# Performance work log

Measured on AMD Instinct MI355X. Metric: run time of the kernel, lower is better.

## Reference

```python
import jax, jax.numpy as jnp
import numpy as np

B, S, H, E, I_E, V = 4, 4096, 1024, 8, 512, 100000


def setup_inputs() -> dict:
    key = jax.random.key(0)
    k0, k1, k2, k3, k4, k5, k6 = jax.random.split(key, 7)
    hidden_states = jax.random.normal(k0, (B, S, H), dtype=jnp.float32)
    token_ids = jax.random.randint(k1, (B, S), 0, V, dtype=jnp.int64)
    mu = jax.random.normal(k2, (B, S, H), dtype=jnp.float32)
    # torch Linear(in,out,bias=False) weight is [out,in]; we store transposed [in,out]
    w_gate = jax.random.normal(k3, (E, H, I_E), dtype=jnp.float32) * 0.02
    w_up = jax.random.normal(k4, (E, H, I_E), dtype=jnp.float32) * 0.02
    w_down = jax.random.normal(k5, (E, I_E, H), dtype=jnp.float32) * 0.02
    # module zero-inits mu_router; use small random so the mu-override path is exercised
    mu_router_w = jax.random.normal(k6, (E, H), dtype=jnp.float32) * 0.02
    return {
        "hidden_states": hidden_states,
        "token_ids": token_ids,
        "mu": mu,
        "w_gate": w_gate,
        "w_up": w_up,
        "w_down": w_down,
        "mu_router_w": mu_router_w,
    }


def reference(hidden_states, token_ids, mu, w_gate, w_up, w_down, mu_router_w):
    num_experts = w_gate.shape[0]
    # deterministic token->expert mapping: token_id % num_experts (after clamp)
    tid = jnp.clip(token_ids, 0, V - 1)
    base_expert_ids = (tid % num_experts).astype(jnp.int32)  # [B,S]
    # mu-guided override: one_hot*10 + mu_logits, argmax
    mu_logits = jnp.einsum("bsh,eh->bse", mu, mu_router_w)
    base_one_hot = jax.nn.one_hot(base_expert_ids, num_experts, dtype=mu_logits.dtype)
    expert_ids = jnp.argmax(base_one_hot * 10.0 + mu_logits, axis=-1)  # [B,S]

    x = hidden_states.reshape(-1, H)          # [T,H], T=B*S
    eid = expert_ids.reshape(-1)              # [T]
    out = jnp.zeros_like(x)
    for e in range(num_experts):
        mask = (eid == e)[:, None]            # [T,1]
        g = x @ w_gate[e]                     # [T,I_E]
        u = x @ w_up[e]                       # [T,I_E]
        y = (jax.nn.silu(g) * u) @ w_down[e]  # [T,H] SwiGLU
        out = out + jnp.where(mask, y, 0.0)
    return out.reshape(hidden_states.shape)
```

## Files before the change

### kernel.cpp

```cpp
#include <hip/hip_runtime.h>
#include <stdint.h>

#define T_TOK   16384
#define H_DIM   1024
#define IE_DIM  512
#define E_NUM   8
#define V_MAX   100000

typedef __attribute__((ext_vector_type(8))) short bf16x8;
typedef __attribute__((ext_vector_type(4))) float f32x4;
typedef unsigned long long ull;

__device__ __forceinline__ unsigned short f2bf(float f) {
  union { float f; unsigned u; } v; v.f = f;
  unsigned r = v.u + 0x7fffu + ((v.u >> 16) & 1u);
  return (unsigned short)(r >> 16);
}

__device__ __forceinline__ void gload16(const void* g, void* l) {
  __builtin_amdgcn_global_load_lds(
      (const __attribute__((address_space(1))) unsigned int*)g,
      (__attribute__((address_space(3))) unsigned int*)(unsigned int)(uintptr_t)l,
      16, 0, 0);
}

__global__ __launch_bounds__(256) void k_route(
    const float* __restrict__ mu, const int* __restrict__ tok,
    const float* __restrict__ mrw, int* __restrict__ eid,
    int* __restrict__ blockCnt) {
  int wv = blockIdx.x * 4 + (threadIdx.x >> 6);
  int t0 = wv * 4;
  int lane = threadIdx.x & 63;
  const float4* mrw4 = (const float4*)mrw;

  __shared__ int cnt[8];
  if (threadIdx.x < 8) cnt[threadIdx.x] = 0;

  float acc[4][E_NUM];
#pragma unroll
  for (int i = 0; i < 4; i++)
#pragma unroll
    for (int e = 0; e < E_NUM; e++) acc[i][e] = 0.f;

#pragma unroll
  for (int j = 0; j < 4; j++) {
    int idx = lane + 64 * j;
    float4 wr[E_NUM];
#pragma unroll
    for (int e = 0; e < E_NUM; e++) wr[e] = mrw4[e * 256 + idx];
#pragma unroll
    for (int i = 0; i < 4; i++) {
      float4 m = ((const float4*)(mu + (size_t)(t0 + i) * H_DIM))[idx];
#pragma unroll
      for (int e = 0; e < E_NUM; e++)
        acc[i][e] += m.x * wr[e].x + m.y * wr[e].y + m.z * wr[e].z + m.w * wr[e].w;
    }
  }
#pragma unroll
  for (int i = 0; i < 4; i++)
#pragma unroll
    for (int e = 0; e < E_NUM; e++)
#pragma unroll
      for (int off = 32; off >= 1; off >>= 1)
        acc[i][e] += __shfl_xor(acc[i][e], off, 64);

  __syncthreads();
#pragma unroll
  for (int i = 0; i < 4; i++) {
    int tv = tok[t0 + i];
    if (tv < 0) tv = 0;
    if (tv > V_MAX - 1) tv = V_MAX - 1;
    int base = tv & 7;
    int best = 0; float bs = -1e30f;
#pragma unroll
    for (int e = 0; e < E_NUM; e++) {
      float s = acc[i][e] + (e == base ? 10.f : 0.f);
      if (s > bs) { bs = s; best = e; }
    }
    if (lane == i) {
      eid[t0 + i] = best;
      atomicAdd(&cnt[best], 1);
    }
  }
  __syncthreads();
  if (threadIdx.x < 8) blockCnt[blockIdx.x * 8 + threadIdx.x] = cnt[threadIdx.x];
}

__global__ __launch_bounds__(1024) void k_scan2(
    const int* __restrict__ blockCnt, int* __restrict__ blockBase,
    int* __restrict__ offsets, int* __restrict__ tileOff) {
  int b = threadIdx.x;
  __shared__ ull s0[1024], s1[1024];
  __shared__ int offL[8];
  const int4* p = (const int4*)(blockCnt + b * 8);
  int4 x0 = p[0], x1 = p[1];
  int c[8] = {x0.x, x0.y, x0.z, x0.w, x1.x, x1.y, x1.z, x1.w};
  ull v0 = (ull)c[0] | ((ull)c[1] << 16) | ((ull)c[2] << 32) | ((ull)c[3] << 48);
  ull v1 = (ull)c[4] | ((ull)c[5] << 16) | ((ull)c[6] << 32) | ((ull)c[7] << 48);
  s0[b] = v0; s1[b] = v1;
  __syncthreads();
  for (int st = 1; st < 1024; st <<= 1) {
    ull a0 = 0, a1 = 0;
    if (b >= st) { a0 = s0[b - st]; a1 = s1[b - st]; }
    __syncthreads();
    v0 += a0; v1 += a1;
    s0[b] = v0; s1[b] = v1;
    __syncthreads();
  }
  if (b == 1023) {
    int tot[8];
#pragma unroll
    for (int e = 0; e < 4; e++) tot[e] = (int)((v0 >> (16 * e)) & 0xFFFF);
#pragma unroll
    for (int e = 0; e < 4; e++) tot[4 + e] = (int)((v1 >> (16 * e)) & 0xFFFF);
    int s = 0, ts = 0;
    for (int e = 0; e < E_NUM; e++) {
      offsets[e] = s; offL[e] = s; tileOff[e] = ts;
      s += tot[e];
      ts += (tot[e] + 127) >> 7;
    }
    offsets[E_NUM] = s; tileOff[E_NUM] = ts;
  }
  __syncthreads();
  int be[8];
#pragma unroll
  for (int e = 0; e < 4; e++)
    be[e] = offL[e] + (int)((v0 >> (16 * e)) & 0xFFFF) - c[e];
#pragma unroll
  for (int e = 0; e < 4; e++)
    be[4 + e] = offL[4 + e] + (int)((v1 >> (16 * e)) & 0xFFFF) - c[4 + e];
  int4* q = (int4*)(blockBase + b * 8);
  q[0] = make_int4(be[0], be[1], be[2], be[3]);
  q[1] = make_int4(be[4], be[5], be[6], be[7]);
}

__global__ __launch_bounds__(256) void k_gather(
    const float* __restrict__ hs, const int* __restrict__ eid,
    const int* __restrict__ blockBase, int* __restrict__ tokofrow,
    unsigned short* __restrict__ Xs) {
  int b = blockIdx.x;
  int tid = threadIdx.x;
  __shared__ int eL[16];
  __shared__ int posL[16];
  if (tid < 16) eL[tid] = eid[b * 16 + tid];
  __syncthreads();
  if (tid < 16) {
    int e = eL[tid];
    int r = 0;
    for (int j = 0; j < tid; j++) r += (eL[j] == e);
    int pos = blockBase[b * 8 + e] + r;
    posL[tid] = pos;
    tokofrow[pos] = b * 16 + tid;
  }
  __syncthreads();
  int w = tid >> 6, lane = tid & 63;
#pragma unroll
  for (int i = 0; i < 4; i++) {
    int li = w * 4 + i;
    int t = b * 16 + li;
    int pos = posL[li];
    const float4* src = (const float4*)(hs + (size_t)t * H_DIM);
    unsigned short* drow = Xs + (size_t)pos * H_DIM;
#pragma unroll
    for (int j = 0; j < 4; j++) {
      float4 v = src[lane + 64 * j];
      ushort4 bb;
      bb.x = f2bf(v.x); bb.y = f2bf(v.y); bb.z = f2bf(v.z); bb.w = f2bf(v.w);
      *(ushort4*)(drow + (lane + 64 * j) * 4) = bb;
    }
  }
}

__global__ __launch_bounds__(256) void k_transpose3(
    const float* __restrict__ wg, const float* __restrict__ wu,
    const float* __restrict__ wd, unsigned short* __restrict__ WgT,
    unsigned short* __restrict__ WuT, unsigned short* __restrict__ WdT) {
  int sel = blockIdx.x >> 10;
  int blk = blockIdx.x & 1023;
  const float* src; unsigned short* dst; int R, C;
  if (sel == 0)      { src = wg; dst = WgT; R = H_DIM; C = IE_DIM; }
  else if (sel == 1) { src = wu; dst = WuT; R = H_DIM; C = IE_DIM; }
  else               { src = wd; dst = WdT; R = IE_DIM; C = H_DIM; }
  int tpe = (R >> 6) * (C >> 6);
  int e = blk / tpe;
  int rem = blk % tpe;
  int tr = rem / (C >> 6);
  int tc = rem % (C >> 6);
  const float* s = src + (size_t)e * R * C;
  unsigned short* d = dst + (size_t)e * R * C;
  __shared__ unsigned short lds[64][72];
  int tid = threadIdx.x;
  int r0 = tid >> 4;
  int c0 = (tid & 15) * 4;
#pragma unroll
  for (int i = 0; i < 4; i++) {
    int r = r0 + i * 16;
    float4 v = *(const float4*)(s + (size_t)(tr * 64 + r) * C + tc * 64 + c0);
    lds[r][c0 + 0] = f2bf(v.x); lds[r][c0 + 1] = f2bf(v.y);
    lds[r][c0 + 2] = f2bf(v.z); lds[r][c0 + 3] = f2bf(v.w);
  }
  __syncthreads();
  int oc = tid >> 2;
  int ob = (tid & 3) * 16;
  unsigned short tmp[16];
#pragma unroll
  for (int i = 0; i < 16; i++) tmp[i] = lds[ob + i][oc];
  uint4* dp = (uint4*)(d + (size_t)(tc * 64 + oc) * R + tr * 64 + ob);
  dp[0] = ((uint4*)tmp)[0];
  dp[1] = ((uint4*)tmp)[1];
}

__global__ __launch_bounds__(512) void k_gemm1(
    const unsigned short* __restrict__ Xs,
    const unsigned short* __restrict__ WgT,
    const unsigned short* __restrict__ WuT,
    unsigned short* __restrict__ Hb,
    const int* __restrict__ offsets, const int* __restrict__ tileOff) {
  int nt = blockIdx.x & 3;
  int mlin = blockIdx.x >> 2;
  if (mlin >= tileOff[E_NUM]) return;
  int e = 0;
#pragma unroll
  for (int i = 1; i < E_NUM; i++)
    if (mlin >= tileOff[i]) e = i;
  int mtile = mlin - tileOff[e];
  int segStart = offsets[e], segEnd = offsets[e + 1];
  int M = segEnd - segStart;

  __shared__ unsigned short Alds[128 * 64];
  __shared__ unsigned short Bglds[128 * 64];
  __shared__ unsigned short Bulds[128 * 64];

  int tid = threadIdx.x;
  int lane = tid & 63;
  int w = tid >> 6;
  int wm = w >> 2;
  int wn = w & 3;

  f32x4 accg[4][2], accu[4][2];
#pragma unroll
  for (int i = 0; i < 4; i++)
#pragma unroll
    for (int j = 0; j < 2; j++) {
      accg[i][j] = (f32x4)(0.f);
      accu[i][j] = (f32x4)(0.f);
    }

  int sr = tid >> 3;
  int sc = tid & 7;
  const unsigned short* Bg =
      WgT + (size_t)e * IE_DIM * H_DIM + (size_t)(nt * 128) * H_DIM;
  const unsigned short* Bu =
      WuT + (size_t)e * IE_DIM * H_DIM + (size_t)(nt * 128) * H_DIM;

  for (int k0 = 0; k0 < H_DIM; k0 += 64) {
#pragma unroll
    for (int p = 0; p < 2; p++) {
      int r = p * 64 + sr;
      int scc = sc ^ (r & 7);
      int grow = mtile * 128 + r;
      if (grow > M - 1) grow = M - 1;
      gload16(Xs + (size_t)(segStart + grow) * H_DIM + k0 + scc * 8,
              (char*)Alds + (p * 512 + tid) * 16);
      gload16(Bg + (size_t)r * H_DIM + k0 + scc * 8,
              (char*)Bglds + (p * 512 + tid) * 16);
      gload16(Bu + (size_t)r * H_DIM + k0 + scc * 8,
              (char*)Bulds + (p * 512 + tid) * 16);
    }
    __syncthreads();
#pragma unroll
    for (int ks = 0; ks < 2; ks++) {
      bf16x8 a[4], bg[2], bu[2];
      int kc = ks * 4 + (lane >> 4);
#pragma unroll
      for (int mf = 0; mf < 4; mf++) {
        int row = wm * 64 + mf * 16 + (lane & 15);
        int byte = row * 128 + ((kc ^ (row & 7)) << 4);
        a[mf] = *(const bf16x8*)((const char*)Alds + byte);
      }
#pragma unroll
      for (int nf = 0; nf < 2; nf++) {
        int row = wn * 32 + nf * 16 + (lane & 15);
        int byte = row * 128 + ((kc ^ (row & 7)) << 4);
        bg[nf] = *(const bf16x8*)((const char*)Bglds + byte);
        bu[nf] = *(const bf16x8*)((const char*)Bulds + byte);
      }
#pragma unroll
      for (int mf = 0; mf < 4; mf++)
#pragma unroll
        for (int nf = 0; nf < 2; nf++) {
          accg[mf][nf] = __builtin_amdgcn_mfma_f32_16x16x32_bf16(
              a[mf], bg[nf], accg[mf][nf], 0, 0, 0);
          accu[mf][nf] = __builtin_amdgcn_mfma_f32_16x16x32_bf16(
              a[mf], bu[nf], accu[mf][nf], 0, 0, 0);
        }
    }
    __syncthreads();
  }

  int rowBase = segStart + mtile * 128 + wm * 64;
#pragma unroll
  for (int mf = 0; mf < 4; mf++)
#pragma unroll
    for (int nf = 0; nf < 2; nf++) {
      int col = nt * 128 + wn * 32 + nf * 16 + (lane & 15);
#pragma unroll
      for (int j = 0; j < 4; j++) {
        int r = rowBase + mf * 16 + (lane >> 4) * 4 + j;
        if (r < segEnd) {
          float g = accg[mf][nf][j];
          float u = accu[mf][nf][j];
          float h = (g / (1.f + __expf(-g))) * u;
          Hb[(size_t)r * IE_DIM + col] = f2bf(h);
        }
      }
    }
}

__global__ __launch_bounds__(512) void k_gemm2(
    const unsigned short* __restrict__ Hb,
    const unsigned short* __restrict__ WdT,
    float* __restrict__ out,
    const int* __restrict__ offsets, const int* __restrict__ tileOff,
    const int* __restrict__ tokofrow) {
  int nt = blockIdx.x & 7;
  int mlin = blockIdx.x >> 3;
  if (mlin >= tileOff[E_NUM]) return;
  int e = 0;
#pragma unroll
  for (int i = 1; i < E_NUM; i++)
    if (mlin >= tileOff[i]) e = i;
  int mtile = mlin - tileOff[e];
  int segStart = offsets[e], segEnd = offsets[e + 1];
  int M = segEnd - segStart;

  __shared__ unsigned short Alds[128 * 64];
  __shared__ unsigned short Blds[128 * 64];

  int tid = threadIdx.x;
  int lane = tid & 63;
  int w = tid >> 6;
  int wm = w >> 2;
  int wn = w & 3;

  f32x4 acc[4][2];
#pragma unroll
  for (int i = 0; i < 4; i++)
#pragma unroll
    for (int j = 0; j < 2; j++) acc[i][j] = (f32x4)(0.f);

  int sr = tid >> 3;
  int sc = tid & 7;
  const unsigned short* Bt =
      WdT + (size_t)e * H_DIM * IE_DIM + (size_t)(nt * 128) * IE_DIM;

  for (int k0 = 0; k0 < IE_DIM; k0 += 64) {
#pragma unroll
    for (int p = 0; p < 2; p++) {
      int r = p * 64 + sr;
      int scc = sc ^ (r & 7);
      int grow = mtile * 128 + r;
      if (grow > M - 1) grow = M - 1;
      gload16(Hb + (size_t)(segStart + grow) * IE_DIM + k0 + scc * 8,
              (char*)Alds + (p * 512 + tid) * 16);
      gload16(Bt + (size_t)r * IE_DIM + k0 + scc * 8,
              (char*)Blds + (p * 512 + tid) * 16);
    }
    __syncthreads();
#pragma unroll
    for (int ks = 0; ks < 2; ks++) {
      bf16x8 a[4], b[2];
      int kc = ks * 4 + (lane >> 4);
#pragma unroll
      for (int mf = 0; mf < 4; mf++) {
        int row = wm * 64 + mf * 16 + (lane & 15);
        int byte = row * 128 + ((kc ^ (row & 7)) << 4);
        a[mf] = *(const bf16x8*)((const char*)Alds + byte);
      }
#pragma unroll
      for (int nf = 0; nf < 2; nf++) {
        int row = wn * 32 + nf * 16 + (lane & 15);
        int byte = row * 128 + ((kc ^ (row & 7)) << 4);
        b[nf] = *(const bf16x8*)((const char*)Blds + byte);
      }
#pragma unroll
      for (int mf = 0; mf < 4; mf++)
#pragma unroll
        for (int nf = 0; nf < 2; nf++)
          acc[mf][nf] = __builtin_amdgcn_mfma_f32_16x16x32_bf16(
              a[mf], b[nf], acc[mf][nf], 0, 0, 0);
    }
    __syncthreads();
  }

  int rowBase = segStart + mtile * 128 + wm * 64;
#pragma unroll
  for (int mf = 0; mf < 4; mf++)
#pragma unroll
    for (int nf = 0; nf < 2; nf++) {
      int col = nt * 128 + wn * 32 + nf * 16 + (lane & 15);
#pragma unroll
      for (int j = 0; j < 4; j++) {
        int r = rowBase + mf * 16 + (lane >> 4) * 4 + j;
        if (r < segEnd) {
          int t = tokofrow[r];
          out[(size_t)t * H_DIM + col] = acc[mf][nf][j];
        }
      }
    }
}

#define WS_XS    ((size_t)0)
#define WS_WGT   ((size_t)33554432)
#define WS_WUT   ((size_t)41943040)
#define WS_WDT   ((size_t)50331648)
#define WS_HB    ((size_t)58720256)
#define WS_EID   ((size_t)75497472)
#define WS_TOK   ((size_t)75563008)
#define WS_OFF   ((size_t)75628544)
#define WS_BC    ((size_t)75629568)
#define WS_BB    ((size_t)75662336)

extern "C" void kernel_launch(void* const* d_in, const int* in_sizes, int n_in,
                              void* d_out, int out_size, void* d_ws, size_t ws_size,
                              hipStream_t stream) {
  const float* hs  = (const float*)d_in[0];
  const int*   tok = (const int*)d_in[1];
  const float* mu  = (const float*)d_in[2];
  const float* wg  = (const float*)d_in[3];
  const float* wu  = (const float*)d_in[4];
  const float* wd  = (const float*)d_in[5];
  const float* mrw = (const float*)d_in[6];
  float* out = (float*)d_out;
  char* ws = (char*)d_ws;

  unsigned short* Xs  = (unsigned short*)(ws + WS_XS);
  unsigned short* WgT = (unsigned short*)(ws + WS_WGT);
  unsigned short* WuT = (unsigned short*)(ws + WS_WUT);
  unsigned short* WdT = (unsigned short*)(ws + WS_WDT);
  unsigned short* Hb  = (unsigned short*)(ws + WS_HB);
  int* eid      = (int*)(ws + WS_EID);
  int* tokofrow = (int*)(ws + WS_TOK);
  int* offsets  = (int*)(ws + WS_OFF);
  int* tileOff  = offsets + 16;
  int* blockCnt = (int*)(ws + WS_BC);
  int* blockBase= (int*)(ws + WS_BB);

  k_route<<<T_TOK / 16, 256, 0, stream>>>(mu, tok, mrw, eid, blockCnt);
  k_transpose3<<<3072, 256, 0, stream>>>(wg, wu, wd, WgT, WuT, WdT);
  k_scan2<<<1, 1024, 0, stream>>>(blockCnt, blockBase, offsets, tileOff);
  k_gather<<<1024, 256, 0, stream>>>(hs, eid, blockBase, tokofrow, Xs);
  k_gemm1<<<135 * 4, 512, 0, stream>>>(Xs, WgT, WuT, Hb, offsets, tileOff);
  k_gemm2<<<135 * 8, 512, 0, stream>>>(Hb, WdT, out, offsets, tileOff, tokofrow);
}
```

Measured before the change: 166.2 us.

## Double-buffer GEMM K-loop with 32-wide tiles and fuse routing with weight transpose

Both expert GEMM kernels now split K into 32-wide steps with two LDS buffers and a new swizzle. Each step issues the async global-to-LDS loads for the next tile before running the MFMAs on the current one, which lets memory latency overlap compute and drops one barrier per step. Separately, the routing and weight-transpose kernels are merged into one launch that picks its job by block index, removing one launch and letting the two run concurrently. In exchange, each K step does less work per barrier, and the merged kernel holds the routing block's register usage across all blocks.

Result: faster. 162.9 us (-2.0%).

```diff
diff --git a/kernel.cpp b/kernel.cpp
--- a/kernel.cpp
+++ b/kernel.cpp
@@ -24,66 +24,105 @@
       16, 0, 0);
 }
 
-__global__ __launch_bounds__(256) void k_route(
+__global__ __launch_bounds__(256) void k_pre(
     const float* __restrict__ mu, const int* __restrict__ tok,
     const float* __restrict__ mrw, int* __restrict__ eid,
-    int* __restrict__ blockCnt) {
-  int wv = blockIdx.x * 4 + (threadIdx.x >> 6);
-  int t0 = wv * 4;
-  int lane = threadIdx.x & 63;
-  const float4* mrw4 = (const float4*)mrw;
-
-  __shared__ int cnt[8];
-  if (threadIdx.x < 8) cnt[threadIdx.x] = 0;
-
-  float acc[4][E_NUM];
-#pragma unroll
-  for (int i = 0; i < 4; i++)
-#pragma unroll
-    for (int e = 0; e < E_NUM; e++) acc[i][e] = 0.f;
-
-#pragma unroll
-  for (int j = 0; j < 4; j++) {
-    int idx = lane + 64 * j;
-    float4 wr[E_NUM];
-#pragma unroll
-    for (int e = 0; e < E_NUM; e++) wr[e] = mrw4[e * 256 + idx];
+    int* __restrict__ blockCnt,
+    const float* __restrict__ wg, const float* __restrict__ wu,
+    const float* __restrict__ wd, unsigned short* __restrict__ WgT,
+    unsigned short* __restrict__ WuT, unsigned short* __restrict__ WdT) {
+  __shared__ unsigned short lds[64][72];
+  int tid = threadIdx.x;
+
+  if (blockIdx.x < 1024) {
+    int* cnt = (int*)&lds[0][0];
+    if (tid < 8) cnt[tid] = 0;
+    int wv = blockIdx.x * 4 + (tid >> 6);
+    int t0 = wv * 4;
+    int lane = tid & 63;
+    const float4* mrw4 = (const float4*)mrw;
+
+    float acc[4][E_NUM];
+#pragma unroll
+    for (int i = 0; i < 4; i++)
+#pragma unroll
+      for (int e = 0; e < E_NUM; e++) acc[i][e] = 0.f;
+
+#pragma unroll
+    for (int j = 0; j < 4; j++) {
+      int idx = lane + 64 * j;
+      float4 wr[E_NUM];
+#pragma unroll
+      for (int e = 0; e < E_NUM; e++) wr[e] = mrw4[e * 256 + idx];
+#pragma unroll
+      for (int i = 0; i < 4; i++) {
+        float4 m = ((const float4*)(mu + (size_t)(t0 + i) * H_DIM))[idx];
+#pragma unroll
+        for (int e = 0; e < E_NUM; e++)
+          acc[i][e] += m.x * wr[e].x + m.y * wr[e].y + m.z * wr[e].z + m.w * wr[e].w;
+      }
+    }
+#pragma unroll
+    for (int i = 0; i < 4; i++)
+#pragma unroll
+      for (int e = 0; e < E_NUM; e++)
+#pragma unroll
+        for (int off = 32; off >= 1; off >>= 1)
+          acc[i][e] += __shfl_xor(acc[i][e], off, 64);
+
+    __syncthreads();
 #pragma unroll
     for (int i = 0; i < 4; i++) {
-      float4 m = ((const float4*)(mu + (size_t)(t0 + i) * H_DIM))[idx];
-#pragma unroll
-      for (int e = 0; e < E_NUM; e++)
-        acc[i][e] += m.x * wr[e].x + m.y * wr[e].y + m.z * wr[e].z + m.w * wr[e].w;
-    }
-  }
-#pragma unroll
-  for (int i = 0; i < 4; i++)
-#pragma unroll
-    for (int e = 0; e < E_NUM; e++)
-#pragma unroll
-      for (int off = 32; off >= 1; off >>= 1)
-        acc[i][e] += __shfl_xor(acc[i][e], off, 64);
-
-  __syncthreads();
-#pragma unroll
-  for (int i = 0; i < 4; i++) {
-    int tv = tok[t0 + i];
-    if (tv < 0) tv = 0;
-    if (tv > V_MAX - 1) tv = V_MAX - 1;
-    int base = tv & 7;
-    int best = 0; float bs = -1e30f;
-#pragma unroll
-    for (int e = 0; e < E_NUM; e++) {
-      float s = acc[i][e] + (e == base ? 10.f : 0.f);
-      if (s > bs) { bs = s; best = e; }
-    }
-    if (lane == i) {
-      eid[t0 + i] = best;
-      atomicAdd(&cnt[best], 1);
-    }
-  }
-  __syncthreads();
-  if (threadIdx.x < 8) blockCnt[blockIdx.x * 8 + threadIdx.x] = cnt[threadIdx.x];
+      int tv = tok[t0 + i];
+      if (tv < 0) tv = 0;
+      if (tv > V_MAX - 1) tv = V_MAX - 1;
+      int base = tv & 7;
+      int best = 0; float bs = -1e30f;
+#pragma unroll
+      for (int e = 0; e < E_NUM; e++) {
+        float s = acc[i][e] + (e == base ? 10.f : 0.f);
+        if (s > bs) { bs = s; best = e; }
+      }
+      if (lane == i) {
+        eid[t0 + i] = best;
+        atomicAdd(&cnt[best], 1);
+      }
+    }
+    __syncthreads();
+    if (tid < 8) blockCnt[blockIdx.x * 8 + tid] = cnt[tid];
+  } else {
+    int sel = (blockIdx.x - 1024) >> 10;
+    int blk = blockIdx.x & 1023;
+    const float* src; unsigned short* dst; int R, C;
+    if (sel == 0)      { src = wg; dst = WgT; R = H_DIM; C = IE_DIM; }
+    else if (sel == 1) { src = wu; dst = WuT; R = H_DIM; C = IE_DIM; }
+    else               { src = wd; dst = WdT; R = IE_DIM; C = H_DIM; }
+    int tpe = (R >> 6) * (C >> 6);
+    int e = blk / tpe;
+    int rem = blk % tpe;
+    int tr = rem / (C >> 6);
+    int tc = rem % (C >> 6);
+    const float* s = src + (size_t)e * R * C;
+    unsigned short* d = dst + (size_t)e * R * C;
+    int r0 = tid >> 4;
+    int c0 = (tid & 15) * 4;
+#pragma unroll
+    for (int i = 0; i < 4; i++) {
+      int r = r0 + i * 16;
+      float4 v = *(const float4*)(s + (size_t)(tr * 64 + r) * C + tc * 64 + c0);
+      lds[r][c0 + 0] = f2bf(v.x); lds[r][c0 + 1] = f2bf(v.y);
+      lds[r][c0 + 2] = f2bf(v.z); lds[r][c0 + 3] = f2bf(v.w);
+    }
+    __syncthreads();
+    int oc = tid >> 2;
+    int ob = (tid & 3) * 16;
+    unsigned short tmp[16];
+#pragma unroll
+    for (int i = 0; i < 16; i++) tmp[i] = lds[ob + i][oc];
+    uint4* dp = (uint4*)(d + (size_t)(tc * 64 + oc) * R + tr * 64 + ob);
+    dp[0] = ((uint4*)tmp)[0];
+    dp[1] = ((uint4*)tmp)[1];
+  }
 }
 
 __global__ __launch_bounds__(1024) void k_scan2(
@@ -171,45 +210,6 @@
   }
 }
 
-__global__ __launch_bounds__(256) void k_transpose3(
-    const float* __restrict__ wg, const float* __restrict__ wu,
-    const float* __restrict__ wd, unsigned short* __restrict__ WgT,
-    unsigned short* __restrict__ WuT, unsigned short* __restrict__ WdT) {
-  int sel = blockIdx.x >> 10;
-  int blk = blockIdx.x & 1023;
-  const float* src; unsigned short* dst; int R, C;
-  if (sel == 0)      { src = wg; dst = WgT; R = H_DIM; C = IE_DIM; }
-  else if (sel == 1) { src = wu; dst = WuT; R = H_DIM; C = IE_DIM; }
-  else               { src = wd; dst = WdT; R = IE_DIM; C = H_DIM; }
-  int tpe = (R >> 6) * (C >> 6);
-  int e = blk / tpe;
-  int rem = blk % tpe;
-  int tr = rem / (C >> 6);
-  int tc = rem % (C >> 6);
-  const float* s = src + (size_t)e * R * C;
-  unsigned short* d = dst + (size_t)e * R * C;
-  __shared__ unsigned short lds[64][72];
-  int tid = threadIdx.x;
-  int r0 = tid >> 4;
-  int c0 = (tid & 15) * 4;
-#pragma unroll
-  for (int i = 0; i < 4; i++) {
-    int r = r0 + i * 16;
-    float4 v = *(const float4*)(s + (size_t)(tr * 64 + r) * C + tc * 64 + c0);
-    lds[r][c0 + 0] = f2bf(v.x); lds[r][c0 + 1] = f2bf(v.y);
-    lds[r][c0 + 2] = f2bf(v.z); lds[r][c0 + 3] = f2bf(v.w);
-  }
-  __syncthreads();
-  int oc = tid >> 2;
-  int ob = (tid & 3) * 16;
-  unsigned short tmp[16];
-#pragma unroll
-  for (int i = 0; i < 16; i++) tmp[i] = lds[ob + i][oc];
-  uint4* dp = (uint4*)(d + (size_t)(tc * 64 + oc) * R + tr * 64 + ob);
-  dp[0] = ((uint4*)tmp)[0];
-  dp[1] = ((uint4*)tmp)[1];
-}
-
 __global__ __launch_bounds__(512) void k_gemm1(
     const unsigned short* __restrict__ Xs,
     const unsigned short* __restrict__ WgT,
@@ -227,9 +227,9 @@
   int segStart = offsets[e], segEnd = offsets[e + 1];
   int M = segEnd - segStart;
 
-  __shared__ unsigned short Alds[128 * 64];
-  __shared__ unsigned short Bglds[128 * 64];
-  __shared__ unsigned short Bulds[128 * 64];
+  __shared__ unsigned short Alds[2][128 * 32];
+  __shared__ unsigned short Bglds[2][128 * 32];
+  __shared__ unsigned short Bulds[2][128 * 32];
 
   int tid = threadIdx.x;
   int lane = tid & 63;
@@ -246,57 +246,65 @@
       accu[i][j] = (f32x4)(0.f);
     }
 
-  int sr = tid >> 3;
-  int sc = tid & 7;
-  const unsigned short* Bg =
-      WgT + (size_t)e * IE_DIM * H_DIM + (size_t)(nt * 128) * H_DIM;
-  const unsigned short* Bu =
-      WuT + (size_t)e * IE_DIM * H_DIM + (size_t)(nt * 128) * H_DIM;
-
-  for (int k0 = 0; k0 < H_DIM; k0 += 64) {
-#pragma unroll
-    for (int p = 0; p < 2; p++) {
-      int r = p * 64 + sr;
-      int scc = sc ^ (r & 7);
-      int grow = mtile * 128 + r;
-      if (grow > M - 1) grow = M - 1;
-      gload16(Xs + (size_t)(segStart + grow) * H_DIM + k0 + scc * 8,
-              (char*)Alds + (p * 512 + tid) * 16);
-      gload16(Bg + (size_t)r * H_DIM + k0 + scc * 8,
-              (char*)Bglds + (p * 512 + tid) * 16);
-      gload16(Bu + (size_t)r * H_DIM + k0 + scc * 8,
-              (char*)Bulds + (p * 512 + tid) * 16);
-    }
-    __syncthreads();
-#pragma unroll
-    for (int ks = 0; ks < 2; ks++) {
-      bf16x8 a[4], bg[2], bu[2];
-      int kc = ks * 4 + (lane >> 4);
-#pragma unroll
-      for (int mf = 0; mf < 4; mf++) {
-        int row = wm * 64 + mf * 16 + (lane & 15);
-        int byte = row * 128 + ((kc ^ (row & 7)) << 4);
-        a[mf] = *(const bf16x8*)((const char*)Alds + byte);
-      }
+  int sr = tid >> 2;
+  int sc = tid & 3;
+  int scc = sc ^ ((sr >> 1) & 3);
+  int grow = mtile * 128 + sr;
+  if (grow > M - 1) grow = M - 1;
+  const unsigned short* Arow = Xs + (size_t)(segStart + grow) * H_DIM + scc * 8;
+  const unsigned short* Bgrow =
+      WgT + (size_t)e * IE_DIM * H_DIM + (size_t)(nt * 128 + sr) * H_DIM + scc * 8;
+  const unsigned short* Burow =
+      WuT + (size_t)e * IE_DIM * H_DIM + (size_t)(nt * 128 + sr) * H_DIM + scc * 8;
+
+#define STAGE1(buf, k0)                                            \
+  {                                                                \
+    gload16(Arow + (k0), (char*)Alds[buf] + tid * 16);             \
+    gload16(Bgrow + (k0), (char*)Bglds[buf] + tid * 16);           \
+    gload16(Burow + (k0), (char*)Bulds[buf] + tid * 16);           \
+  }
+
+  int kc = lane >> 4;
+  int arow[4], brow[2];
+#pragma unroll
+  for (int mf = 0; mf < 4; mf++) arow[mf] = wm * 64 + mf * 16 + (lane & 15);
+#pragma unroll
+  for (int nf = 0; nf < 2; nf++) brow[nf] = wn * 32 + nf * 16 + (lane & 15);
+
+  STAGE1(0, 0);
+  __syncthreads();
+
+  const int NT = H_DIM / 32;
+  int cur = 0;
+  for (int t = 0; t < NT; t++) {
+    if (t + 1 < NT) STAGE1(cur ^ 1, (t + 1) * 32);
+    bf16x8 a[4], bg[2], bu[2];
+#pragma unroll
+    for (int mf = 0; mf < 4; mf++) {
+      int row = arow[mf];
+      int byte = row * 64 + ((kc ^ ((row >> 1) & 3)) << 4);
+      a[mf] = *(const bf16x8*)((const char*)Alds[cur] + byte);
+    }
+#pragma unroll
+    for (int nf = 0; nf < 2; nf++) {
+      int row = brow[nf];
+      int byte = row * 64 + ((kc ^ ((row >> 1) & 3)) << 4);
+      bg[nf] = *(const bf16x8*)((const char*)Bglds[cur] + byte);
+      bu[nf] = *(const bf16x8*)((const char*)Bulds[cur] + byte);
+    }
+#pragma unroll
+    for (int mf = 0; mf < 4; mf++)
 #pragma unroll
       for (int nf = 0; nf < 2; nf++) {
-        int row = wn * 32 + nf * 16 + (lane & 15);
-        int byte = row * 128 + ((kc ^ (row & 7)) << 4);
-        bg[nf] = *(const bf16x8*)((const char*)Bglds + byte);
-        bu[nf] = *(const bf16x8*)((const char*)Bulds + byte);
-      }
-#pragma unroll
-      for (int mf = 0; mf < 4; mf++)
-#pragma unroll
-        for (int nf = 0; nf < 2; nf++) {
-          accg[mf][nf] = __builtin_amdgcn_mfma_f32_16x16x32_bf16(
-              a[mf], bg[nf], accg[mf][nf], 0, 0, 0);
-          accu[mf][nf] = __builtin_amdgcn_mfma_f32_16x16x32_bf16(
-              a[mf], bu[nf], accu[mf][nf], 0, 0, 0);
-        }
-    }
-    __syncthreads();
-  }
+        accg[mf][nf] = __builtin_amdgcn_mfma_f32_16x16x32_bf16(
+            a[mf], bg[nf], accg[mf][nf], 0, 0, 0);
+        accu[mf][nf] = __builtin_amdgcn_mfma_f32_16x16x32_bf16(
+            a[mf], bu[nf], accu[mf][nf], 0, 0, 0);
+      }
+    __syncthreads();
+    cur ^= 1;
+  }
+#undef STAGE1
 
   int rowBase = segStart + mtile * 128 + wm * 64;
 #pragma unroll
@@ -334,8 +342,8 @@
   int segStart = offsets[e], segEnd = offsets[e + 1];
   int M = segEnd - segStart;
 
-  __shared__ unsigned short Alds[128 * 64];
-  __shared__ unsigned short Blds[128 * 64];
+  __shared__ unsigned short Alds[2][128 * 32];
+  __shared__ unsigned short Blds[2][128 * 32];
 
   int tid = threadIdx.x;
   int lane = tid & 63;
@@ -349,49 +357,58 @@
 #pragma unroll
     for (int j = 0; j < 2; j++) acc[i][j] = (f32x4)(0.f);
 
-  int sr = tid >> 3;
-  int sc = tid & 7;
-  const unsigned short* Bt =
-      WdT + (size_t)e * H_DIM * IE_DIM + (size_t)(nt * 128) * IE_DIM;
-
-  for (int k0 = 0; k0 < IE_DIM; k0 += 64) {
-#pragma unroll
-    for (int p = 0; p < 2; p++) {
-      int r = p * 64 + sr;
-      int scc = sc ^ (r & 7);
-      int grow = mtile * 128 + r;
-      if (grow > M - 1) grow = M - 1;
-      gload16(Hb + (size_t)(segStart + grow) * IE_DIM + k0 + scc * 8,
-              (char*)Alds + (p * 512 + tid) * 16);
-      gload16(Bt + (size_t)r * IE_DIM + k0 + scc * 8,
-              (char*)Blds + (p * 512 + tid) * 16);
-    }
-    __syncthreads();
-#pragma unroll
-    for (int ks = 0; ks < 2; ks++) {
-      bf16x8 a[4], b[2];
-      int kc = ks * 4 + (lane >> 4);
-#pragma unroll
-      for (int mf = 0; mf < 4; mf++) {
-        int row = wm * 64 + mf * 16 + (lane & 15);
-        int byte = row * 128 + ((kc ^ (row & 7)) << 4);
-        a[mf] = *(const bf16x8*)((const char*)Alds + byte);
-      }
-#pragma unroll
-      for (int nf = 0; nf < 2; nf++) {
-        int row = wn * 32 + nf * 16 + (lane & 15);
-        int byte = row * 128 + ((kc ^ (row & 7)) << 4);
-        b[nf] = *(const bf16x8*)((const char*)Blds + byte);
-      }
-#pragma unroll
-      for (int mf = 0; mf < 4; mf++)
-#pragma unroll
-        for (int nf = 0; nf < 2; nf++)
-          acc[mf][nf] = __builtin_amdgcn_mfma_f32_16x16x32_bf16(
-              a[mf], b[nf], acc[mf][nf], 0, 0, 0);
-    }
-    __syncthreads();
-  }
+  int sr = tid >> 2;
+  int sc = tid & 3;
+  int scc = sc ^ ((sr >> 1) & 3);
+  int grow = mtile * 128 + sr;
+  if (grow > M - 1) grow = M - 1;
+  const unsigned short* Arow = Hb + (size_t)(segStart + grow) * IE_DIM + scc * 8;
+  const unsigned short* Brow =
+      WdT + (size_t)e * H_DIM * IE_DIM + (size_t)(nt * 128 + sr) * IE_DIM + scc * 8;
+
+#define STAGE2(buf, k0)                                            \
+  {                                                                \
+    gload16(Arow + (k0), (char*)Alds[buf] + tid * 16);             \
+    gload16(Brow + (k0), (char*)Blds[buf] + tid * 16);             \
+  }
+
+  int kc = lane >> 4;
+  int arow[4], brow[2];
+#pragma unroll
+  for (int mf = 0; mf < 4; mf++) arow[mf] = wm * 64 + mf * 16 + (lane & 15);
+#pragma unroll
+  for (int nf = 0; nf < 2; nf++) brow[nf] = wn * 32 + nf * 16 + (lane & 15);
+
+  STAGE2(0, 0);
+  __syncthreads();
+
+  const int NT = IE_DIM / 32;
+  int cur = 0;
+  for (int t = 0; t < NT; t++) {
+    if (t + 1 < NT) STAGE2(cur ^ 1, (t + 1) * 32);
+    bf16x8 a[4], b[2];
+#pragma unroll
+    for (int mf = 0; mf < 4; mf++) {
+      int row = arow[mf];
+      int byte = row * 64 + ((kc ^ ((row >> 1) & 3)) << 4);
+      a[mf] = *(const bf16x8*)((const char*)Alds[cur] + byte);
+    }
+#pragma unroll
+    for (int nf = 0; nf < 2; nf++) {
+      int row = brow[nf];
+      int byte = row * 64 + ((kc ^ ((row >> 1) & 3)) << 4);
+      b[nf] = *(const bf16x8*)((const char*)Blds[cur] + byte);
+    }
+#pragma unroll
+    for (int mf = 0; mf < 4; mf++)
+#pragma unroll
+      for (int nf = 0; nf < 2; nf++)
+        acc[mf][nf] = __builtin_amdgcn_mfma_f32_16x16x32_bf16(
+            a[mf], b[nf], acc[mf][nf], 0, 0, 0);
+    __syncthreads();
+    cur ^= 1;
+  }
+#undef STAGE2
 
   int rowBase = segStart + mtile * 128 + wm * 64;
 #pragma unroll
@@ -446,8 +463,8 @@
   int* blockCnt = (int*)(ws + WS_BC);
   int* blockBase= (int*)(ws + WS_BB);
 
-  k_route<<<T_TOK / 16, 256, 0, stream>>>(mu, tok, mrw, eid, blockCnt);
-  k_transpose3<<<3072, 256, 0, stream>>>(wg, wu, wd, WgT, WuT, WdT);
+  k_pre<<<4096, 256, 0, stream>>>(mu, tok, mrw, eid, blockCnt,
+                                  wg, wu, wd, WgT, WuT, WdT);
   k_scan2<<<1, 1024, 0, stream>>>(blockCnt, blockBase, offsets, tileOff);
   k_gather<<<1024, 256, 0, stream>>>(hs, eid, blockBase, tokofrow, Xs);
   k_gemm1<<<135 * 4, 512, 0, stream>>>(Xs, WgT, WuT, Hb, offsets, tileOff);
```
